# Optimization experiments

Measured on AMD Instinct MI355X. Metric: run time of the kernel, lower is better.

The kernel has to match this reference:

```python
import jax, jax.numpy as jnp
import numpy as np

D_MODEL = 1024
HEADS = 16
D_HEAD = D_MODEL // HEADS
LN_EPS = 1e-6


def setup_inputs() -> dict:
    key = jax.random.key(0)
    ks = jax.random.split(key, 7)
    B, S = 4, 2048
    scale = 1.0 / np.sqrt(D_MODEL)
    return {
        "q": jax.random.normal(ks[0], (B, S, D_MODEL), jnp.float32),
        "k": jax.random.normal(ks[1], (B, S, D_MODEL), jnp.float32),
        "v": jax.random.normal(ks[2], (B, S, D_MODEL), jnp.float32),
        "Wq": jax.random.normal(ks[3], (D_MODEL, D_MODEL), jnp.float32) * scale,
        "Wk": jax.random.normal(ks[4], (D_MODEL, D_MODEL), jnp.float32) * scale,
        "Wv": jax.random.normal(ks[5], (D_MODEL, D_MODEL), jnp.float32) * scale,
        "Wo": jax.random.normal(ks[6], (D_MODEL, D_MODEL), jnp.float32) * scale,
        "ln_gamma": jnp.ones((D_MODEL,), jnp.float32),
        "ln_beta": jnp.zeros((D_MODEL,), jnp.float32),
    }


def reference(q, k, v, Wq, Wk, Wv, Wo, ln_gamma, ln_beta):
    B, S, _ = q.shape
    residual = q
    # torch Linear (no bias): y = x @ W.T
    qh = (q @ Wq.T).reshape(B, S, HEADS, D_HEAD).transpose(0, 2, 1, 3)
    kh = (k @ Wk.T).reshape(B, S, HEADS, D_HEAD).transpose(0, 2, 1, 3)
    vh = (v @ Wv.T).reshape(B, S, HEADS, D_HEAD).transpose(0, 2, 1, 3)
    # scaled dot-product attention (no mask, dropout=0)
    att = jnp.einsum("bhsd,bhtd->bhst", qh, kh) / jnp.sqrt(jnp.float32(D_HEAD))
    att = jax.nn.softmax(att, axis=-1)
    ctx = jnp.einsum("bhst,bhtd->bhsd", att, vh)  # (B,H,S,Dh)
    ctx = ctx.transpose(0, 2, 1, 3).reshape(B, S, D_MODEL)
    out = ctx @ Wo.T
    out = out + residual
    # LayerNorm, eps=1e-6
    mu = out.mean(axis=-1, keepdims=True)
    var = out.var(axis=-1, keepdims=True)
    out = (out - mu) * jax.lax.rsqrt(var + LN_EPS) * ln_gamma + ln_beta
    return out
```

## Files before the change

### kernel.cpp

```cpp
#include <hip/hip_runtime.h>
#include <hip/hip_bf16.h>

#define DEVI __device__ __forceinline__

typedef unsigned int u32;
typedef unsigned short u16;
typedef __bf16 bf16_t;
typedef bf16_t bf16x8 __attribute__((ext_vector_type(8)));
typedef bf16_t bf16x4 __attribute__((ext_vector_type(4)));
typedef float f32x4 __attribute__((ext_vector_type(4)));
typedef u32 u32x4 __attribute__((ext_vector_type(4)));
typedef u32 u32x2 __attribute__((ext_vector_type(2)));

DEVI u16 f2bf(float f) {
    u32 u = __builtin_bit_cast(u32, f);
    u = (u + 0x7FFFu + ((u >> 16) & 1u)) >> 16;
    return (u16)u;
}

DEVI u32 pack2bf(float lo, float hi) {
#if __has_builtin(__builtin_amdgcn_cvt_pk_bf16_f32)
    typedef __bf16 bf16x2_t __attribute__((ext_vector_type(2)));
    return __builtin_bit_cast(u32, __builtin_amdgcn_cvt_pk_bf16_f32(lo, hi));
#else
    return (u32)f2bf(lo) | ((u32)f2bf(hi) << 16);
#endif
}

DEVI float fast_exp2(float x) { return __builtin_amdgcn_exp2f(x); }

typedef __attribute__((address_space(3))) u32 as3_u32;
typedef __attribute__((address_space(1))) u32 as1_u32;

DEVI void gld_lds16(const u16* gsrc, u16* ldst) {
    __builtin_amdgcn_global_load_lds((as1_u32*)gsrc, (as3_u32*)ldst, 16, 0, 0);
}

struct CastArgs {
    const float* src[7];
    u16* dst[7];
    int n[7];
};

__global__ __launch_bounds__(256) void cast_kernel(CastArgs a) {
    int z = blockIdx.y;
    int i = (blockIdx.x * 256 + threadIdx.x) * 8;
    if (i >= a.n[z]) return;
    const float* s = a.src[z] + i;
    float4 f0 = ((const float4*)s)[0];
    float4 f1 = ((const float4*)s)[1];
    u32x4 o;
    o.x = pack2bf(f0.x, f0.y);
    o.y = pack2bf(f0.z, f0.w);
    o.z = pack2bf(f1.x, f1.y);
    o.w = pack2bf(f1.z, f1.w);
    *(u32x4*)(a.dst[z] + i) = o;
}

DEVI void gemm_core(const u16* __restrict__ Ag, const u16* __restrict__ Wg,
                    u16* As, u16* Bs, f32x4 acc[4][4],
                    int tid, int mw, int nw, int q, int cl)
{
    const int K = 1024;
    for (int k0 = 0; k0 < K; k0 += 64) {
        if (k0) __syncthreads();
        #pragma unroll
        for (int pass = 0; pass < 4; ++pass) {
            int id = pass * 256 + tid;
            int r = id >> 3, cp = id & 7, cg = cp ^ (r & 7);
            gld_lds16(Ag + (size_t)r * K + k0 + cg * 8, &As[id * 8]);
            gld_lds16(Wg + (size_t)r * K + k0 + cg * 8, &Bs[id * 8]);
        }
        __syncthreads();
        #pragma unroll
        for (int kh = 0; kh < 2; ++kh) {
            bf16x8 af[4], bfr[4];
            #pragma unroll
            for (int i = 0; i < 4; ++i) {
                int R = mw + i * 16 + cl;
                af[i] = *(const bf16x8*)&As[R * 64 + (((kh * 4 + q) ^ (cl & 7)) * 8)];
            }
            #pragma unroll
            for (int j = 0; j < 4; ++j) {
                int R = nw + j * 16 + cl;
                bfr[j] = *(const bf16x8*)&Bs[R * 64 + (((kh * 4 + q) ^ (cl & 7)) * 8)];
            }
            #pragma unroll
            for (int i = 0; i < 4; ++i)
                #pragma unroll
                for (int j = 0; j < 4; ++j)
                    acc[i][j] = __builtin_amdgcn_mfma_f32_16x16x32_bf16(af[i], bfr[j], acc[i][j], 0, 0, 0);
        }
    }
}

struct QKVArgs { const u16* A[3]; const u16* W[3]; u16* out[3]; };

__global__ __launch_bounds__(256) void qkv_gemm(QKVArgs ga) {
    __shared__ __align__(16) u16 As[128 * 64];
    __shared__ __align__(16) u16 Bs[128 * 64];
    int z = blockIdx.z;
    int tid = threadIdx.x;
    int lane = tid & 63, w = tid >> 6;
    int q = lane >> 4, cl = lane & 15;
    int m0 = blockIdx.y * 128, n0 = blockIdx.x * 128;
    int mw = (w >> 1) * 64, nw = (w & 1) * 64;

    f32x4 acc[4][4] = {};
    const u16* Ag = ga.A[z] + (size_t)m0 * 1024;
    const u16* Wg = ga.W[z] + (size_t)n0 * 1024;
    gemm_core(Ag, Wg, As, Bs, acc, tid, mw, nw, q, cl);

    u16* outb = ga.out[z];
    if (z == 0) {
        const float SC = 0.125f * 1.44269504088896340736f;
        #pragma unroll
        for (int i = 0; i < 4; ++i) {
            int row = m0 + mw + i * 16 + q * 4;
            #pragma unroll
            for (int j = 0; j < 4; ++j) {
                int col = n0 + nw + j * 16 + cl;
                #pragma unroll
                for (int r = 0; r < 4; ++r)
                    outb[(size_t)(row + r) * 1024 + col] = f2bf(acc[i][j][r] * SC);
            }
        }
    } else if (z == 1) {
        #pragma unroll
        for (int i = 0; i < 4; ++i) {
            int row = m0 + mw + i * 16 + q * 4;
            #pragma unroll
            for (int j = 0; j < 4; ++j) {
                int col = n0 + nw + j * 16 + cl;
                #pragma unroll
                for (int r = 0; r < 4; ++r)
                    outb[(size_t)(row + r) * 1024 + col] = f2bf(acc[i][j][r]);
            }
        }
    } else {
        #pragma unroll
        for (int i = 0; i < 4; ++i) {
            int mrow = m0 + mw + i * 16 + q * 4;
            int bb = mrow >> 11, s = mrow & 2047;
            #pragma unroll
            for (int j = 0; j < 4; ++j) {
                int n = n0 + nw + j * 16 + cl;
                ushort4 pk;
                pk.x = f2bf(acc[i][j][0]); pk.y = f2bf(acc[i][j][1]);
                pk.z = f2bf(acc[i][j][2]); pk.w = f2bf(acc[i][j][3]);
                *(ushort4*)&outb[(size_t)(bb * 1024 + n) * 2048 + s] = pk;
            }
        }
    }
}

__global__ __launch_bounds__(256) void gemm_wo(
    const u16* __restrict__ A, const u16* __restrict__ W,
    float* __restrict__ outf, const float* __restrict__ resid)
{
    __shared__ __align__(16) u16 As[128 * 64];
    __shared__ __align__(16) u16 Bs[128 * 64];
    int tid = threadIdx.x;
    int lane = tid & 63, w = tid >> 6;
    int q = lane >> 4, cl = lane & 15;
    int m0 = blockIdx.y * 128, n0 = blockIdx.x * 128;
    int mw = (w >> 1) * 64, nw = (w & 1) * 64;

    f32x4 acc[4][4] = {};
    const u16* Ag = A + (size_t)m0 * 1024;
    const u16* Wg = W + (size_t)n0 * 1024;
    gemm_core(Ag, Wg, As, Bs, acc, tid, mw, nw, q, cl);

    #pragma unroll
    for (int i = 0; i < 4; ++i) {
        int row = m0 + mw + i * 16 + q * 4;
        #pragma unroll
        for (int j = 0; j < 4; ++j) {
            int col = n0 + nw + j * 16 + cl;
            #pragma unroll
            for (int r = 0; r < 4; ++r) {
                size_t idx = (size_t)(row + r) * 1024 + col;
                outf[idx] = acc[i][j][r] + resid[idx];
            }
        }
    }
}


DEVI int kperm(int r) {
    return (r & 96) | ((r & 12) << 1) | ((r & 16) >> 2) | (r & 3);
}

__global__ __launch_bounds__(256, 4) void attn_kernel(
    const u16* __restrict__ Qp, const u16* __restrict__ Kp,
    const u16* __restrict__ Vt, u16* __restrict__ ctx)
{
    __shared__ __align__(16) u16 Ks[128 * 64];
    __shared__ __align__(16) u16 Vs[64 * 128];

    int tid = threadIdx.x;
    int lane = tid & 63, w = tid >> 6;
    int q = lane >> 4, cl = lane & 15;
    int bh = blockIdx.y, b = bh >> 4, h = bh & 15;
    int qt = blockIdx.x;

    const u16* Qg = Qp + (size_t)(b * 2048 + qt * 128) * 1024 + h * 64;
    const u16* Kg = Kp + (size_t)(b * 2048) * 1024 + h * 64;
    const u16* Vg = Vt + (size_t)(b * 1024 + h * 64) * 2048;

    bf16x8 aq[2][2];
    #pragma unroll
    for (int tr = 0; tr < 2; ++tr)
        #pragma unroll
        for (int kk = 0; kk < 2; ++kk)
            aq[tr][kk] = *(const bf16x8*)&Qg[(size_t)(w * 32 + tr * 16 + cl) * 1024 + kk * 32 + q * 8];

    u32x4 ou; ou.x = 0x3F803F80u; ou.y = 0x3F803F80u; ou.z = 0x3F803F80u; ou.w = 0x3F803F80u;
    const bf16x8 ones = __builtin_bit_cast(bf16x8, ou);

    f32x4 oacc[2][4] = {};
    f32x4 lacc[2] = {};

    for (int kt = 0; kt < 16; ++kt) {
        __syncthreads();
        #pragma unroll
        for (int p = 0; p < 4; ++p) {
            int cid = p * 256 + tid;
            int r = cid >> 3, cp = cid & 7, cg = cp ^ (r & 7);
            gld_lds16(Kg + (size_t)(kt * 128 + kperm(r)) * 1024 + cg * 8, &Ks[cid * 8]);
        }
        #pragma unroll
        for (int p = 0; p < 4; ++p) {
            int cid = p * 256 + tid;
            int r = cid >> 4, cp = cid & 15, cg = cp ^ (r & 15);
            gld_lds16(Vg + (size_t)r * 2048 + kt * 128 + cg * 8, &Vs[cid * 8]);
        }
        __syncthreads();

        bf16x8 pb[2][4];
        #pragma unroll
        for (int t = 0; t < 4; ++t) {
            int krA = t * 32 + cl, krB = t * 32 + 16 + cl;
            bf16x8 ka0 = *(const bf16x8*)&Ks[krA * 64 + ((q ^ (cl & 7)) * 8)];
            bf16x8 ka1 = *(const bf16x8*)&Ks[krA * 64 + (((4 + q) ^ (cl & 7)) * 8)];
            bf16x8 kb0 = *(const bf16x8*)&Ks[krB * 64 + ((q ^ (cl & 7)) * 8)];
            bf16x8 kb1 = *(const bf16x8*)&Ks[krB * 64 + (((4 + q) ^ (cl & 7)) * 8)];
            #pragma unroll
            for (int tr = 0; tr < 2; ++tr) {
                f32x4 sA = {0.f, 0.f, 0.f, 0.f};
                f32x4 sB = {0.f, 0.f, 0.f, 0.f};
                __builtin_amdgcn_s_setprio(1);
                sA = __builtin_amdgcn_mfma_f32_16x16x32_bf16(ka0, aq[tr][0], sA, 0, 0, 0);
                sA = __builtin_amdgcn_mfma_f32_16x16x32_bf16(ka1, aq[tr][1], sA, 0, 0, 0);
                sB = __builtin_amdgcn_mfma_f32_16x16x32_bf16(kb0, aq[tr][0], sB, 0, 0, 0);
                sB = __builtin_amdgcn_mfma_f32_16x16x32_bf16(kb1, aq[tr][1], sB, 0, 0, 0);
                __builtin_amdgcn_s_setprio(0);
                u32x4 pk;
                pk.x = pack2bf(fast_exp2(sA[0]), fast_exp2(sA[1]));
                pk.y = pack2bf(fast_exp2(sA[2]), fast_exp2(sA[3]));
                pk.z = pack2bf(fast_exp2(sB[0]), fast_exp2(sB[1]));
                pk.w = pack2bf(fast_exp2(sB[2]), fast_exp2(sB[3]));
                pb[tr][t] = __builtin_bit_cast(bf16x8, pk);
            }
        }

        #pragma unroll
        for (int t = 0; t < 4; ++t) {
            #pragma unroll
            for (int td = 0; td < 4; ++td) {
                int d = td * 16 + cl;
                bf16x8 bv = *(const bf16x8*)&Vs[d * 128 + (((t * 4 + q) ^ cl) * 8)];
                __builtin_amdgcn_s_setprio(1);
                oacc[0][td] = __builtin_amdgcn_mfma_f32_16x16x32_bf16(pb[0][t], bv, oacc[0][td], 0, 0, 0);
                oacc[1][td] = __builtin_amdgcn_mfma_f32_16x16x32_bf16(pb[1][t], bv, oacc[1][td], 0, 0, 0);
                __builtin_amdgcn_s_setprio(0);
            }
            __builtin_amdgcn_s_setprio(1);
            lacc[0] = __builtin_amdgcn_mfma_f32_16x16x32_bf16(pb[0][t], ones, lacc[0], 0, 0, 0);
            lacc[1] = __builtin_amdgcn_mfma_f32_16x16x32_bf16(pb[1][t], ones, lacc[1], 0, 0, 0);
            __builtin_amdgcn_s_setprio(0);
        }
    }

    u16* Cg = ctx + (size_t)(b * 2048 + qt * 128) * 1024 + h * 64;
    #pragma unroll
    for (int tr = 0; tr < 2; ++tr) {
        #pragma unroll
        for (int r = 0; r < 4; ++r) {
            float ir = 1.f / lacc[tr][r];
            int srow = w * 32 + tr * 16 + q * 4 + r;
            #pragma unroll
            for (int td = 0; td < 4; ++td)
                Cg[(size_t)srow * 1024 + td * 16 + cl] = f2bf(oacc[tr][td][r] * ir);
        }
    }
}

__global__ __launch_bounds__(256) void ln_kernel(float* __restrict__ out,
    const float* __restrict__ gamma, const float* __restrict__ beta)
{
    int r = blockIdx.x, tid = threadIdx.x;
    int lane = tid & 63, w = tid >> 6;
    float* x = out + (size_t)r * 1024;
    float4 v = *(const float4*)&x[tid * 4];
    float s = v.x + v.y + v.z + v.w;
    float ss = v.x * v.x + v.y * v.y + v.z * v.z + v.w * v.w;
    #pragma unroll
    for (int off = 1; off < 64; off <<= 1) {
        s += __shfl_xor(s, off, 64);
        ss += __shfl_xor(ss, off, 64);
    }
    __shared__ float red[8];
    if (lane == 0) { red[w] = s; red[4 + w] = ss; }
    __syncthreads();
    s = red[0] + red[1] + red[2] + red[3];
    ss = red[4] + red[5] + red[6] + red[7];
    float mean = s * (1.f / 1024.f);
    float var = ss * (1.f / 1024.f) - mean * mean;
    float rstd = rsqrtf(var + 1e-6f);
    float4 g = *(const float4*)&gamma[tid * 4];
    float4 bt = *(const float4*)&beta[tid * 4];
    float4 y;
    y.x = (v.x - mean) * rstd * g.x + bt.x;
    y.y = (v.y - mean) * rstd * g.y + bt.y;
    y.z = (v.z - mean) * rstd * g.z + bt.z;
    y.w = (v.w - mean) * rstd * g.w + bt.w;
    *(float4*)&x[tid * 4] = y;
}

extern "C" void kernel_launch(void* const* d_in, const int* in_sizes, int n_in,
                              void* d_out, int out_size, void* d_ws, size_t ws_size,
                              hipStream_t stream) {
    const float* q  = (const float*)d_in[0];
    const float* k  = (const float*)d_in[1];
    const float* v  = (const float*)d_in[2];
    const float* Wq = (const float*)d_in[3];
    const float* Wk = (const float*)d_in[4];
    const float* Wv = (const float*)d_in[5];
    const float* Wo = (const float*)d_in[6];
    const float* gamma = (const float*)d_in[7];
    const float* beta  = (const float*)d_in[8];
    float* out = (float*)d_out;

    u16* qb  = (u16*)d_ws;
    u16* kb  = qb + 8388608;
    u16* vb  = kb + 8388608;
    u16* Wqb = vb + 8388608;
    u16* Wkb = Wqb + 1048576;
    u16* Wvb = Wkb + 1048576;
    u16* Wob = Wvb + 1048576;
    u16* Qp  = Wob + 1048576;
    u16* Kp  = Qp + 8388608;
    u16* Vtb = Kp + 8388608;
    u16* ctx = Vtb + 8388608;

    CastArgs ca;
    ca.src[0] = q;  ca.src[1] = k;  ca.src[2] = v;
    ca.src[3] = Wq; ca.src[4] = Wk; ca.src[5] = Wv; ca.src[6] = Wo;
    ca.dst[0] = qb;  ca.dst[1] = kb;  ca.dst[2] = vb;
    ca.dst[3] = Wqb; ca.dst[4] = Wkb; ca.dst[5] = Wvb; ca.dst[6] = Wob;
    ca.n[0] = ca.n[1] = ca.n[2] = 8388608;
    ca.n[3] = ca.n[4] = ca.n[5] = ca.n[6] = 1048576;

    cast_kernel<<<dim3(4096, 7), 256, 0, stream>>>(ca);

    QKVArgs ga;
    ga.A[0] = qb;  ga.A[1] = kb;  ga.A[2] = vb;
    ga.W[0] = Wqb; ga.W[1] = Wkb; ga.W[2] = Wvb;
    ga.out[0] = Qp; ga.out[1] = Kp; ga.out[2] = Vtb;
    qkv_gemm<<<dim3(8, 64, 3), 256, 0, stream>>>(ga);

    attn_kernel<<<dim3(16, 64), 256, 0, stream>>>(Qp, Kp, Vtb, ctx);

    gemm_wo<<<dim3(8, 64), 256, 0, stream>>>(ctx, Wob, out, q);

    ln_kernel<<<8192, 256, 0, stream>>>(out, gamma, beta);
}
```

Measured before the change: 381.2 us.

## Double-buffer K/V LDS tiles in attention kernel to overlap loads with MFMA

Splits the K and V shared-memory tiles into two buffers and issues the direct-to-LDS loads for the next key tile before computing on the current one. A single waitcnt plus barrier per iteration replaces the two syncthreads. The intent is to hide global-load latency behind the QK and PV MFMA work. LDS use doubles and the occupancy hint drops from 4 to 2 blocks per CU, so there is less latency hiding from other waves.

```diff
diff --git a/kernel.cpp b/kernel.cpp
--- a/kernel.cpp
+++ b/kernel.cpp
@@ -191,12 +191,12 @@
     return (r & 96) | ((r & 12) << 1) | ((r & 16) >> 2) | (r & 3);
 }
 
-__global__ __launch_bounds__(256, 4) void attn_kernel(
+__global__ __launch_bounds__(256, 2) void attn_kernel(
     const u16* __restrict__ Qp, const u16* __restrict__ Kp,
     const u16* __restrict__ Vt, u16* __restrict__ ctx)
 {
-    __shared__ __align__(16) u16 Ks[128 * 64];
-    __shared__ __align__(16) u16 Vs[64 * 128];
+    __shared__ __align__(16) u16 Ks[2][128 * 64];
+    __shared__ __align__(16) u16 Vs[2][64 * 128];
 
     int tid = threadIdx.x;
     int lane = tid & 63, w = tid >> 6;
@@ -221,30 +221,42 @@
     f32x4 oacc[2][4] = {};
     f32x4 lacc[2] = {};
 
-    for (int kt = 0; kt < 16; ++kt) {
-        __syncthreads();
+    auto stage = [&](int kt, int bufsel) {
         #pragma unroll
         for (int p = 0; p < 4; ++p) {
             int cid = p * 256 + tid;
             int r = cid >> 3, cp = cid & 7, cg = cp ^ (r & 7);
-            gld_lds16(Kg + (size_t)(kt * 128 + kperm(r)) * 1024 + cg * 8, &Ks[cid * 8]);
+            gld_lds16(Kg + (size_t)(kt * 128 + kperm(r)) * 1024 + cg * 8, &Ks[bufsel][cid * 8]);
         }
         #pragma unroll
         for (int p = 0; p < 4; ++p) {
             int cid = p * 256 + tid;
             int r = cid >> 4, cp = cid & 15, cg = cp ^ (r & 15);
-            gld_lds16(Vg + (size_t)r * 2048 + kt * 128 + cg * 8, &Vs[cid * 8]);
-        }
-        __syncthreads();
+            gld_lds16(Vg + (size_t)r * 2048 + kt * 128 + cg * 8, &Vs[bufsel][cid * 8]);
+        }
+    };
+
+    stage(0, 0);
+    asm volatile("s_waitcnt vmcnt(0)" ::: "memory");
+    __builtin_amdgcn_s_barrier();
+    __builtin_amdgcn_sched_barrier(0);
+
+    for (int kt = 0; kt < 16; ++kt) {
+        int cur = kt & 1;
+        if (kt < 15) stage(kt + 1, cur ^ 1);
+        __builtin_amdgcn_sched_barrier(0);
+
+        const u16* KsC = &Ks[cur][0];
+        const u16* VsC = &Vs[cur][0];
 
         bf16x8 pb[2][4];
         #pragma unroll
         for (int t = 0; t < 4; ++t) {
             int krA = t * 32 + cl, krB = t * 32 + 16 + cl;
-            bf16x8 ka0 = *(const bf16x8*)&Ks[krA * 64 + ((q ^ (cl & 7)) * 8)];
-            bf16x8 ka1 = *(const bf16x8*)&Ks[krA * 64 + (((4 + q) ^ (cl & 7)) * 8)];
-            bf16x8 kb0 = *(const bf16x8*)&Ks[krB * 64 + ((q ^ (cl & 7)) * 8)];
-            bf16x8 kb1 = *(const bf16x8*)&Ks[krB * 64 + (((4 + q) ^ (cl & 7)) * 8)];
+            bf16x8 ka0 = *(const bf16x8*)&KsC[krA * 64 + ((q ^ (cl & 7)) * 8)];
+            bf16x8 ka1 = *(const bf16x8*)&KsC[krA * 64 + (((4 + q) ^ (cl & 7)) * 8)];
+            bf16x8 kb0 = *(const bf16x8*)&KsC[krB * 64 + ((q ^ (cl & 7)) * 8)];
+            bf16x8 kb1 = *(const bf16x8*)&KsC[krB * 64 + (((4 + q) ^ (cl & 7)) * 8)];
             #pragma unroll
             for (int tr = 0; tr < 2; ++tr) {
                 f32x4 sA = {0.f, 0.f, 0.f, 0.f};
@@ -269,7 +281,7 @@
             #pragma unroll
             for (int td = 0; td < 4; ++td) {
                 int d = td * 16 + cl;
-                bf16x8 bv = *(const bf16x8*)&Vs[d * 128 + (((t * 4 + q) ^ cl) * 8)];
+                bf16x8 bv = *(const bf16x8*)&VsC[d * 128 + (((t * 4 + q) ^ cl) * 8)];
                 __builtin_amdgcn_s_setprio(1);
                 oacc[0][td] = __builtin_amdgcn_mfma_f32_16x16x32_bf16(pb[0][t], bv, oacc[0][td], 0, 0, 0);
                 oacc[1][td] = __builtin_amdgcn_mfma_f32_16x16x32_bf16(pb[1][t], bv, oacc[1][td], 0, 0, 0);
@@ -280,6 +292,10 @@
             lacc[1] = __builtin_amdgcn_mfma_f32_16x16x32_bf16(pb[1][t], ones, lacc[1], 0, 0, 0);
             __builtin_amdgcn_s_setprio(0);
         }
+
+        asm volatile("s_waitcnt vmcnt(0)" ::: "memory");
+        __builtin_amdgcn_s_barrier();
+        __builtin_amdgcn_sched_barrier(0);
     }
 
     u16* Cg = ctx + (size_t)(b * 2048 + qt * 128) * 1024 + h * 64;
```

After: 370.6 us. 2.8% less time.
